# Kernel optimization log

Measured on AMD Instinct MI355X. Metric: run time of the kernel, lower is better.

The kernel has to match this reference:

```python
import jax, jax.numpy as jnp
import numpy as np

N = 50000      # total packed nodes
E = 1600000    # edges (no self loops; layers add them)
G = 64         # graphs in the batch
F_IN = 24      # raw node feature dim
D = 64         # hidden dim
H = 4          # attention heads
C = D // H     # 16 channels per head
L = 3          # GAT layers
NEG = 0.2      # LeakyReLU negative slope (GATv2 default)
EPS = 1e-5     # LayerNorm eps


def setup_inputs() -> dict:
    key = jax.random.key(0)
    ks = jax.random.split(key, 16)
    x = jax.random.normal(ks[0], (N, F_IN), jnp.float32)
    src = jax.random.randint(ks[1], (E,), 0, N)
    dst = jax.random.randint(ks[2], (E,), 0, N)
    dst = jnp.where(dst == src, (dst + 1) % N, dst)  # keep edge list self-loop free
    edge_index = jnp.stack([src, dst]).astype(jnp.int32)
    batch = jnp.sort(jax.random.randint(ks[3], (N,), 0, G)).astype(jnp.int32)
    s = 0.1
    return dict(
        x=x, edge_index=edge_index, batch=batch,
        w_in=jax.random.normal(ks[4], (F_IN, D), jnp.float32) * s,
        b_in=jnp.zeros((D,), jnp.float32),
        w_l=jax.random.normal(ks[5], (L, D, D), jnp.float32) * s,
        b_l=jnp.zeros((L, D), jnp.float32),
        w_r=jax.random.normal(ks[6], (L, D, D), jnp.float32) * s,
        b_r=jnp.zeros((L, D), jnp.float32),
        att=jax.random.normal(ks[7], (L, H, C), jnp.float32) * s,
        b_gat=jnp.zeros((L, D), jnp.float32),
        ln_g=jnp.ones((L, D), jnp.float32),
        ln_b=jnp.zeros((L, D), jnp.float32),
        w_g1=jax.random.normal(ks[8], (D, D // 2), jnp.float32) * s,
        b_g1=jnp.zeros((D // 2,), jnp.float32),
        w_g2=jax.random.normal(ks[9], (D // 2, 1), jnp.float32) * s,
        b_g2=jnp.zeros((1,), jnp.float32),
        w_out=jax.random.normal(ks[10], (D, D), jnp.float32) * s,
        b_out=jnp.zeros((D,), jnp.float32),
    )


def _layernorm(h, g, b):
    m = h.mean(-1, keepdims=True)
    v = ((h - m) ** 2).mean(-1, keepdims=True)
    return (h - m) * jax.lax.rsqrt(v + EPS) * g + b


def _gatv2(h, src, dst, wl, bl, wr, br, att, bg):
    n = h.shape[0]
    xl = (h @ wl + bl).reshape(n, H, C)   # source transform
    xr = (h @ wr + br).reshape(n, H, C)   # target transform
    # edge scores: att . leaky_relu(xl[j] + xr[i])  -> [E', H]
    e = jnp.sum(jax.nn.leaky_relu(xl[src] + xr[dst], NEG) * att, axis=-1)
    emax = jax.ops.segment_max(e, dst, num_segments=n)
    ex = jnp.exp(e - emax[dst])
    denom = jax.ops.segment_sum(ex, dst, num_segments=n)
    alpha = ex / denom[dst]               # segment softmax over incoming edges
    out = jax.ops.segment_sum(alpha[:, :, None] * xl[src], dst, num_segments=n)
    return out.reshape(n, D) + bg


def reference(x, edge_index, batch, w_in, b_in, w_l, b_l, w_r, b_r, att, b_gat,
              ln_g, ln_b, w_g1, b_g1, w_g2, b_g2, w_out, b_out):
    n = x.shape[0]
    loops = jnp.arange(n, dtype=edge_index.dtype)
    src = jnp.concatenate([edge_index[0], loops])  # add self loops once
    dst = jnp.concatenate([edge_index[1], loops])
    h = jax.nn.relu(x @ w_in + b_in)
    for i in range(L):
        res = h
        h = _gatv2(h, src, dst, w_l[i], b_l[i], w_r[i], b_r[i], att[i], b_gat[i])
        h = _layernorm(h + res, ln_g[i], ln_b[i])
        if i < L - 1:
            h = jax.nn.relu(h)
    # GlobalAttention pooling: gate MLP -> per-graph softmax -> weighted sum
    gate = jax.nn.relu(h @ w_g1 + b_g1) @ w_g2 + b_g2  # [N, 1]
    gmax = jax.ops.segment_max(gate, batch, num_segments=G)
    ge = jnp.exp(gate - gmax[batch])
    gs = jax.ops.segment_sum(ge, batch, num_segments=G)
    a = ge / jnp.where(gs > 0, gs, 1.0)[batch]
    emb = jax.ops.segment_sum(a * h, batch, num_segments=G)  # [G, D]
    return jax.nn.relu(emb @ w_out + b_out)
```

## Files before the change

### kernel.cpp

```cpp
#include <hip/hip_runtime.h>

#define NEGS   0.2f
#define LN_EPS 1e-5f
#define BSH    7
#define BN     128
#define TILE   4096
#define LOG2E  1.44269504f

typedef const float* __restrict__ fp;
typedef _Float16 v2h __attribute__((ext_vector_type(2)));
typedef _Float16 v8h __attribute__((ext_vector_type(8)));
typedef float    v4f __attribute__((ext_vector_type(4)));

__device__ __forceinline__ v2h u2h(unsigned u){ union{unsigned u; v2h h;} c; c.u = u; return c.h; }
__device__ __forceinline__ unsigned h2u(v2h h){ union{v2h h; unsigned u;} c; c.h = h; return c.u; }

template<int CTRL>
__device__ __forceinline__ float dppadd(float x){
  int y = __builtin_amdgcn_update_dpp(0, __float_as_int(x), CTRL, 0xF, 0xF, true);
  return x + __int_as_float(y);
}
__device__ __forceinline__ float hsum8(float s){
  s = dppadd<0xB1>(s);
  s = dppadd<0x4E>(s);
  s = dppadd<0x141>(s);
  return s;
}
__device__ __forceinline__ float edge_w(v2h v, v2h xrv, v2h att2, float negm8){
  v2h t = v + xrv;
  t = __builtin_elementwise_max(t, t * (_Float16)NEGS);
  float s = hsum8(__builtin_amdgcn_fdot2(t, att2, negm8, false));
  return __builtin_amdgcn_exp2f(s);
}

__global__ __launch_bounds__(256) void k_in(fp x, fp w, fp b, float* __restrict__ h,
                                            unsigned* __restrict__ h16, int N){
  __shared__ float ws[24*64];
  __shared__ float bs[64];
  __shared__ float xs[4][24];
  int tid = threadIdx.x;
  for (int i = tid; i < 24*64; i += 256) ws[i] = w[i];
  if (tid < 64) bs[tid] = b[tid];
  int r = tid >> 6, c = tid & 63;
  int row = blockIdx.x*4 + r;
  if (c < 24 && row < N) xs[r][c] = x[row*24 + c];
  __syncthreads();
  float acc = bs[c];
  #pragma unroll
  for (int k = 0; k < 24; ++k) acc = fmaf(xs[r][k], ws[k*64 + c], acc);
  float y = fmaxf(acc, 0.f);
  float y1 = __shfl_down(y, 1);
  if (row < N){
    h[(size_t)row*64 + c] = y;
    if (!(c & 1)){
      v2h p; p.x = (_Float16)y; p.y = (_Float16)y1;
      h16[(size_t)row*32 + (c >> 1)] = h2u(p);
    }
  }
}

__global__ __launch_bounds__(256) void k_wprep(fp w_l, fp w_r, _Float16* __restrict__ wf){
  int lm = blockIdx.x;
  const float* src = ((lm & 1) ? w_r : w_l) + (lm >> 1)*4096;
  _Float16* dst = wf + lm*4096;
  for (int d = threadIdx.x; d < 4096; d += 256){
    int j = d & 7, l = (d >> 3) & 63, kc = (d >> 9) & 1, nt = d >> 10;
    int k = kc*32 + (l >> 4)*8 + j;
    int n = nt*16 + (l & 15);
    dst[d] = (_Float16)src[k*64 + n];
  }
}

__global__ __launch_bounds__(256) void t_hist(const int* __restrict__ dstA, int* __restrict__ counts,
                                              int E, int K, int ntiles){
  __shared__ int hist[512];
  int t = blockIdx.x, tid = threadIdx.x;
  for (int i = tid; i < K; i += 256) hist[i] = 0;
  __syncthreads();
  int e0 = t*TILE, e1 = min(e0 + TILE, E);
  for (int e = e0 + tid; e < e1; e += 256)
    atomicAdd(&hist[dstA[e] >> BSH], 1);
  __syncthreads();
  for (int i = tid; i < K; i += 256) counts[i*ntiles + t] = hist[i];
}

__global__ __launch_bounds__(512) void s_scan_tiles(int* __restrict__ counts, int* __restrict__ btotal,
                                                    int ntiles){
  __shared__ int s[512];
  int b = blockIdx.x, tid = threadIdx.x;
  int v = (tid < ntiles) ? counts[b*ntiles + tid] : 0;
  s[tid] = v;
  __syncthreads();
  for (int off = 1; off < 512; off <<= 1){
    int t = (tid >= off) ? s[tid - off] : 0;
    __syncthreads();
    s[tid] += t;
    __syncthreads();
  }
  if (tid < ntiles) counts[b*ntiles + tid] = s[tid] - v;
  if (tid == 511) btotal[b] = s[511];
}

__global__ __launch_bounds__(512) void s_scan_buckets(const int* __restrict__ btotal,
                                                      int* __restrict__ bbase, int K, int E){
  __shared__ int s[512];
  int tid = threadIdx.x;
  int v = (tid < K) ? btotal[tid] : 0;
  s[tid] = v;
  __syncthreads();
  for (int off = 1; off < 512; off <<= 1){
    int t = (tid >= off) ? s[tid - off] : 0;
    __syncthreads();
    s[tid] += t;
    __syncthreads();
  }
  if (tid < K) bbase[tid] = s[tid] - v;
  if (tid == 0) bbase[K] = E;
}

__global__ __launch_bounds__(256) void t_scatter(const int* __restrict__ srcA, const int* __restrict__ dstA,
                                                 const int* __restrict__ counts, const int* __restrict__ bbase,
                                                 unsigned* __restrict__ packed, int E, int K, int ntiles){
  __shared__ int gb[512];
  __shared__ int cur[512];
  int t = blockIdx.x, tid = threadIdx.x;
  for (int i = tid; i < K; i += 256){
    gb[i] = bbase[i] + counts[i*ntiles + t];
    cur[i] = 0;
  }
  __syncthreads();
  int e0 = t*TILE, e1 = min(e0 + TILE, E);
  for (int e = e0 + tid; e < e1; e += 256){
    int d = dstA[e], sv = srcA[e];
    int b = d >> BSH;
    int p = atomicAdd(&cur[b], 1);
    packed[gb[b] + p] = ((unsigned)(d & (BN-1)) << 25) | (unsigned)sv;
  }
}

__global__ __launch_bounds__(256) void k_fine(const unsigned* __restrict__ packed, const int* __restrict__ bbase,
                                              int* __restrict__ row_ptr, int* __restrict__ col, int N, int K){
  __shared__ int hist[BN];
  __shared__ int excl[BN];
  int b = blockIdx.x, tid = threadIdx.x;
  int node0 = b << BSH;
  int e_base = bbase[b], e_end = bbase[b+1];
  if (tid < BN) hist[tid] = 0;
  __syncthreads();
  for (int e = e_base + tid; e < e_end; e += 256)
    atomicAdd(&hist[packed[e] >> 25], 1);
  __syncthreads();
  int v = (tid < BN) ? hist[tid] : 0;
  if (tid < BN) excl[tid] = v;
  __syncthreads();
  for (int off = 1; off < BN; off <<= 1){
    int t2 = 0;
    if (tid < BN && tid >= off) t2 = excl[tid - off];
    __syncthreads();
    if (tid < BN) excl[tid] += t2;
    __syncthreads();
  }
  int nn = min(BN, N - node0);
  if (tid < nn) row_ptr[node0 + tid] = e_base + excl[tid] - v;
  if (b == K-1 && tid == 0) row_ptr[N] = e_end;
  if (tid < BN) hist[tid] = excl[tid] - v;
  __syncthreads();
  for (int e = e_base + tid; e < e_end; e += 256){
    unsigned u = packed[e];
    int dl = u >> 25;
    int p = atomicAdd(&hist[dl], 1);
    col[e_base + p] = (int)(u & 0x1FFFFFFu);
  }
}

__global__ __launch_bounds__(256) void k_xfm(const unsigned* __restrict__ h16,
                                             const _Float16* __restrict__ wf,
                                             fp blg, fp brg,
                                             unsigned* __restrict__ xl16, unsigned* __restrict__ xr16, int N){
  int tid = threadIdx.x, wave = tid >> 6, lane = tid & 63;
  int quad = lane >> 4, ln = lane & 15;
  int m0 = blockIdx.x*64 + wave*16;
  if (m0 >= N) return;
  int m = m0 + ln;
  bool mv = m < N;
  v8h a0 = {}, a1 = {};
  if (mv){
    a0 = *(const v8h*)&h16[(size_t)m*32 + quad*4];
    a1 = *(const v8h*)&h16[(size_t)m*32 + 16 + quad*4];
  }
  #pragma unroll
  for (int mat = 0; mat < 2; ++mat){
    const _Float16* wb = wf + mat*4096;
    fp bias = mat ? brg : blg;
    unsigned* dst = mat ? xr16 : xl16;
    #pragma unroll
    for (int nt = 0; nt < 4; ++nt){
      v8h b0 = *(const v8h*)&wb[nt*1024 + lane*8];
      v8h b1 = *(const v8h*)&wb[nt*1024 + 512 + lane*8];
      float bv = bias[nt*16 + ln];
      v4f acc = {bv, bv, bv, bv};
      acc = __builtin_amdgcn_mfma_f32_16x16x32_f16(a0, b0, acc, 0, 0, 0);
      acc = __builtin_amdgcn_mfma_f32_16x16x32_f16(a1, b1, acc, 0, 0, 0);
      #pragma unroll
      for (int r = 0; r < 4; ++r){
        float partner = __shfl_xor(acc[r], 1);
        int node = m0 + quad*4 + r;
        if (!(lane & 1) && node < N){
          v2h p; p.x = (_Float16)acc[r]; p.y = (_Float16)partner;
          dst[(size_t)node*32 + nt*8 + (ln >> 1)] = h2u(p);
        }
      }
    }
  }
}

__global__ __launch_bounds__(256) void k_gat(const unsigned* __restrict__ xl16, const unsigned* __restrict__ xr16,
                                             float* __restrict__ h, unsigned* __restrict__ h16,
                                             const int* __restrict__ row_ptr, const int* __restrict__ col,
                                             fp att, fp bg, fp lng, fp lnb, int N, int do_relu){
  int lane = threadIdx.x & 63;
  int node = blockIdx.x*4 + (threadIdx.x >> 6);
  if (node >= N) return;
  int l = lane & 31;
  bool lower = lane < 32;
  int off = lower ? 0 : 1;
  v2h att2; att2.x = (_Float16)(att[2*l] * LOG2E); att2.y = (_Float16)(att[2*l+1] * LOG2E);
  v2h xrv = u2h(xr16[(size_t)node*32 + l]);
  v2h xlv = u2h(xl16[(size_t)node*32 + l]);
  v2h ts = xlv + xrv;
  ts = __builtin_elementwise_max(ts, ts * (_Float16)NEGS);
  const float m = hsum8(__builtin_amdgcn_fdot2(ts, att2, 0.f, false));
  const float negm8 = m * -0.125f;
  float den0 = lower ? 1.f : 0.f, den1 = 0.f, den2 = 0.f, den3 = 0.f;
  float a0x = lower ? (float)xlv.x : 0.f, a0y = lower ? (float)xlv.y : 0.f;
  float a1x = 0.f, a1y = 0.f, a2x = 0.f, a2y = 0.f, a3x = 0.f, a3y = 0.f;
  int e = row_ptr[node], e1 = row_ptr[node+1];
  for (; e + 8 <= e1; e += 8){
    int j0 = col[e+off], j1 = col[e+2+off], j2 = col[e+4+off], j3 = col[e+6+off];
    v2h v0 = u2h(xl16[(size_t)j0*32 + l]);
    v2h v1 = u2h(xl16[(size_t)j1*32 + l]);
    v2h v2 = u2h(xl16[(size_t)j2*32 + l]);
    v2h v3 = u2h(xl16[(size_t)j3*32 + l]);
    float w0 = edge_w(v0, xrv, att2, negm8);
    float w1 = edge_w(v1, xrv, att2, negm8);
    float w2 = edge_w(v2, xrv, att2, negm8);
    float w3 = edge_w(v3, xrv, att2, negm8);
    den0 += w0; a0x = fmaf(w0, (float)v0.x, a0x); a0y = fmaf(w0, (float)v0.y, a0y);
    den1 += w1; a1x = fmaf(w1, (float)v1.x, a1x); a1y = fmaf(w1, (float)v1.y, a1y);
    den2 += w2; a2x = fmaf(w2, (float)v2.x, a2x); a2y = fmaf(w2, (float)v2.y, a2y);
    den3 += w3; a3x = fmaf(w3, (float)v3.x, a3x); a3y = fmaf(w3, (float)v3.y, a3y);
  }
  for (; e + 2 <= e1; e += 2){
    int j0 = col[e+off];
    v2h v0 = u2h(xl16[(size_t)j0*32 + l]);
    float w0 = edge_w(v0, xrv, att2, negm8);
    den0 += w0; a0x = fmaf(w0, (float)v0.x, a0x); a0y = fmaf(w0, (float)v0.y, a0y);
  }
  if (e < e1){
    int j0 = col[e];
    v2h v0 = u2h(xl16[(size_t)j0*32 + l]);
    float w0 = edge_w(v0, xrv, att2, negm8);
    if (!lower) w0 = 0.f;
    den0 += w0; a0x = fmaf(w0, (float)v0.x, a0x); a0y = fmaf(w0, (float)v0.y, a0y);
  }
  float den = (den0 + den1) + (den2 + den3);
  float ax = (a0x + a1x) + (a2x + a3x);
  float ay = (a0y + a1y) + (a2y + a3y);
  den += __shfl_xor(den, 32);
  ax  += __shfl_xor(ax, 32);
  ay  += __shfl_xor(ay, 32);
  float inv = 1.f / den;
  float2 bg2 = *(const float2*)&bg[2*l];
  float2 h2  = *(const float2*)&h[(size_t)node*64 + 2*l];
  float ox = ax*inv + bg2.x + h2.x;
  float oy = ay*inv + bg2.y + h2.y;
  float sl = ox + oy;
  #pragma unroll
  for (int o = 1; o < 32; o <<= 1) sl += __shfl_xor(sl, o);
  float mean = sl * (1.f/64.f);
  float dx = ox - mean, dy = oy - mean;
  float vsl = dx*dx + dy*dy;
  #pragma unroll
  for (int o = 1; o < 32; o <<= 1) vsl += __shfl_xor(vsl, o);
  float rs = rsqrtf(vsl * (1.f/64.f) + LN_EPS);
  float2 lg2 = *(const float2*)&lng[2*l];
  float2 lb2 = *(const float2*)&lnb[2*l];
  float yx = dx*rs*lg2.x + lb2.x;
  float yy = dy*rs*lg2.y + lb2.y;
  if (do_relu){ yx = fmaxf(yx, 0.f); yy = fmaxf(yy, 0.f); }
  if (lower){
    float2 y2; y2.x = yx; y2.y = yy;
    *(float2*)&h[(size_t)node*64 + 2*l] = y2;
    v2h p; p.x = (_Float16)yx; p.y = (_Float16)yy;
    h16[(size_t)node*32 + l] = h2u(p);
  }
}

__global__ __launch_bounds__(256) void k_gate(const float* __restrict__ h, fp w1, fp b1, fp w2, fp b2,
                                              float* __restrict__ gate, int N){
  __shared__ float w1s[2048];
  __shared__ float hrow[16][64];
  int tid = threadIdx.x;
  for (int i = tid*4; i < 2048; i += 1024) *(float4*)&w1s[i] = *(const float4*)&w1[i];
  int base = blockIdx.x*16;
  int nrows = min(16, N - base);
  int lim = nrows*64;
  for (int i = tid*4; i < lim; i += 1024)
    *(float4*)&hrow[0][i] = *(const float4*)&h[(size_t)base*64 + i];
  __syncthreads();
  int wave = tid >> 6, lane = tid & 63;
  int j = lane & 31, half = lane >> 5;
  float b1v = b1[j], w2v = w2[j], b2v = b2[0];
  int k0 = half*32;
  #pragma unroll
  for (int it = 0; it < 4; ++it){
    int r = wave*4 + it;
    int node = base + r;
    if (node >= N) break;
    float s = 0.f;
    #pragma unroll 8
    for (int k = k0; k < k0 + 32; ++k) s = fmaf(hrow[r][k], w1s[k*32 + j], s);
    s += __shfl_xor(s, 32);
    float hid = fmaxf(s + b1v, 0.f);
    float contrib = (half == 0) ? hid * w2v : 0.f;
    #pragma unroll
    for (int o = 1; o < 64; o <<= 1) contrib += __shfl_xor(contrib, o);
    if (lane == 0) gate[node] = contrib + b2v;
  }
}

__global__ __launch_bounds__(256) void k_gmax(const float* __restrict__ gate, const int* __restrict__ batch,
                                              float* __restrict__ gmax, float* __restrict__ gsum,
                                              float* __restrict__ embsum, int N){
  int g = blockIdx.x, tid = threadIdx.x;
  if (tid < 64) embsum[g*64 + tid] = 0.f;
  if (tid == 64) gsum[g] = 0.f;
  int lo = 0, hi = N;
  while (lo < hi){ int mid = (lo + hi) >> 1; if (batch[mid] < g) lo = mid + 1; else hi = mid; }
  int start = lo;
  hi = N;
  while (lo < hi){ int mid = (lo + hi) >> 1; if (batch[mid] < g + 1) lo = mid + 1; else hi = mid; }
  int end = lo;
  float m = -3.4e38f;
  for (int i = start + tid; i < end; i += 256) m = fmaxf(m, gate[i]);
  #pragma unroll
  for (int o = 1; o < 64; o <<= 1) m = fmaxf(m, __shfl_xor(m, o));
  __shared__ float ws[4];
  if ((tid & 63) == 0) ws[tid >> 6] = m;
  __syncthreads();
  if (tid == 0) gmax[g] = fmaxf(fmaxf(ws[0], ws[1]), fmaxf(ws[2], ws[3]));
}

__global__ __launch_bounds__(256) void k_emb(const float* __restrict__ h, const float* __restrict__ gate,
                                             const int* __restrict__ batch, const float* __restrict__ gmax,
                                             float* __restrict__ gsum, float* __restrict__ embsum, int N){
  int lane = threadIdx.x & 63;
  int wv = blockIdx.x*4 + (threadIdx.x >> 6);
  int s = wv*64;
  if (s >= N) return;
  int e = min(s + 64, N);
  int cur = batch[s];
  float gm = gmax[cur];
  float acc = 0.f, asum = 0.f;
  for (int i = s; i < e; ++i){
    int g = batch[i];
    if (g != cur){
      atomicAdd(&embsum[cur*64 + lane], acc);
      if (lane == 0) atomicAdd(&gsum[cur], asum);
      acc = 0.f; asum = 0.f; cur = g; gm = gmax[g];
    }
    float a = __expf(gate[i] - gm);
    acc = fmaf(a, h[(size_t)i*64 + lane], acc);
    asum += a;
  }
  atomicAdd(&embsum[cur*64 + lane], acc);
  if (lane == 0) atomicAdd(&gsum[cur], asum);
}

__global__ __launch_bounds__(64) void k_out(const float* __restrict__ embsum, const float* __restrict__ gsum,
                                            fp w_out, fp b_out, float* __restrict__ out, int G){
  int g = blockIdx.x, lane = threadIdx.x;
  __shared__ float emb[64];
  float gs = gsum[g];
  float inv = (gs > 0.f) ? 1.f/gs : 1.f;
  emb[lane] = embsum[g*64 + lane] * inv;
  __syncthreads();
  float o2 = b_out[lane];
  #pragma unroll 8
  for (int d = 0; d < 64; ++d) o2 = fmaf(emb[d], w_out[d*64 + lane], o2);
  out[g*64 + lane] = fmaxf(o2, 0.f);
}

extern "C" void kernel_launch(void* const* d_in, const int* in_sizes, int n_in,
                              void* d_out, int out_size, void* d_ws, size_t ws_size,
                              hipStream_t stream) {
  const int N = in_sizes[0] / 24;
  const int E = in_sizes[1] / 2;
  const int G = out_size / 64;
  const int K = (N + BN - 1) >> BSH;
  const int ntiles = (E + TILE - 1) / TILE;

  fp x      = (fp)d_in[0];
  const int* edge  = (const int*)d_in[1];
  const int* batch = (const int*)d_in[2];
  fp w_in   = (fp)d_in[3];
  fp b_in   = (fp)d_in[4];
  fp w_l    = (fp)d_in[5];
  fp b_l    = (fp)d_in[6];
  fp w_r    = (fp)d_in[7];
  fp b_r    = (fp)d_in[8];
  fp att    = (fp)d_in[9];
  fp b_gat  = (fp)d_in[10];
  fp ln_g   = (fp)d_in[11];
  fp ln_b   = (fp)d_in[12];
  fp w_g1   = (fp)d_in[13];
  fp b_g1   = (fp)d_in[14];
  fp w_g2   = (fp)d_in[15];
  fp b_g2   = (fp)d_in[16];
  fp w_out  = (fp)d_in[17];
  fp b_out  = (fp)d_in[18];
  float* out = (float*)d_out;

  char* wp = (char*)d_ws;
  auto alloc = [&](size_t bytes) -> char* {
    char* p = wp; wp += (bytes + 255) & ~(size_t)255; return p;
  };
  float*    h       = (float*)    alloc((size_t)N*64*sizeof(float));
  unsigned* h16     = (unsigned*) alloc((size_t)N*32*sizeof(unsigned));
  unsigned* xl16    = (unsigned*) alloc((size_t)N*32*sizeof(unsigned));
  unsigned* xr16    = (unsigned*) alloc((size_t)N*32*sizeof(unsigned));
  int*      col     = (int*)      alloc((size_t)E*sizeof(int));
  unsigned* packed  = (unsigned*) alloc((size_t)E*sizeof(unsigned));
  int*      counts  = (int*)      alloc((size_t)K*ntiles*sizeof(int));
  int*      btotal  = (int*)      alloc((size_t)K*sizeof(int));
  int*      bbase   = (int*)      alloc((size_t)(K+1)*sizeof(int));
  int*      row_ptr = (int*)      alloc((size_t)(N+1)*sizeof(int));
  float*    gate    = (float*)    alloc((size_t)N*sizeof(float));
  float*    gmax    = (float*)    alloc((size_t)G*sizeof(float));
  float*    gsum    = (float*)    alloc((size_t)(G + G*64)*sizeof(float));
  float*    embsum  = gsum + G;
  _Float16* wf      = (_Float16*) alloc((size_t)3*2*4096*sizeof(_Float16));

  const int* srcA = edge;
  const int* dstA = edge + E;

  k_in<<<(N + 3)/4, 256, 0, stream>>>(x, w_in, b_in, h, h16, N);
  k_wprep<<<6, 256, 0, stream>>>(w_l, w_r, wf);

  t_hist<<<ntiles, 256, 0, stream>>>(dstA, counts, E, K, ntiles);
  s_scan_tiles<<<K, 512, 0, stream>>>(counts, btotal, ntiles);
  s_scan_buckets<<<1, 512, 0, stream>>>(btotal, bbase, K, E);
  t_scatter<<<ntiles, 256, 0, stream>>>(srcA, dstA, counts, bbase, packed, E, K, ntiles);
  k_fine<<<K, 256, 0, stream>>>(packed, bbase, row_ptr, col, N, K);

  for (int i = 0; i < 3; ++i){
    k_xfm<<<(N + 63)/64, 256, 0, stream>>>(h16, wf + i*8192, b_l + i*64, b_r + i*64,
                                           xl16, xr16, N);
    k_gat<<<(N + 3)/4, 256, 0, stream>>>(xl16, xr16, h, h16, row_ptr, col,
                                         att + i*64, b_gat + i*64, ln_g + i*64, ln_b + i*64,
                                         N, i < 2 ? 1 : 0);
  }
  k_gate<<<(N + 15)/16, 256, 0, stream>>>(h, w_g1, b_g1, w_g2, b_g2, gate, N);
  k_gmax<<<G, 256, 0, stream>>>(gate, batch, gmax, gsum, embsum, N);
  k_emb<<<(N + 255)/256, 256, 0, stream>>>(h, gate, batch, gmax, gsum, embsum, N);
  k_out<<<G, 64, 0, stream>>>(embsum, gsum, w_out, b_out, out, G);
}
```

Before: 384.9 us.

## Fuse prologue kernels, merge scans, and fuse gate pooling into one pass

The input projection, per-tile destination histogram, weight fp16 repacking and zeroing of pooling accumulators are merged into one launch that branches on block index. The two prefix-scan kernels become one, where the last block to finish (found through an atomic counter) does the bucket scan. The gate MLP, per-graph max and weighted embedding sum become one kernel that reuses the h rows already in shared memory and drops the max subtraction from the softmax. Fewer launches and less global traffic are the aim; the risks are possible exp overflow for large gates and reliance on threadfence plus the atomic counter being correct for the scan handoff.

After: 486.5 us. +26.4%, slower.

```diff
diff --git a/kernel.cpp b/kernel.cpp
--- a/kernel.cpp
+++ b/kernel.cpp
@@ -33,60 +33,67 @@
   return __builtin_amdgcn_exp2f(s);
 }
 
-__global__ __launch_bounds__(256) void k_in(fp x, fp w, fp b, float* __restrict__ h,
-                                            unsigned* __restrict__ h16, int N){
-  __shared__ float ws[24*64];
-  __shared__ float bs[64];
-  __shared__ float xs[4][24];
-  int tid = threadIdx.x;
-  for (int i = tid; i < 24*64; i += 256) ws[i] = w[i];
-  if (tid < 64) bs[tid] = b[tid];
-  int r = tid >> 6, c = tid & 63;
-  int row = blockIdx.x*4 + r;
-  if (c < 24 && row < N) xs[r][c] = x[row*24 + c];
-  __syncthreads();
-  float acc = bs[c];
-  #pragma unroll
-  for (int k = 0; k < 24; ++k) acc = fmaf(xs[r][k], ws[k*64 + c], acc);
-  float y = fmaxf(acc, 0.f);
-  float y1 = __shfl_down(y, 1);
-  if (row < N){
-    h[(size_t)row*64 + c] = y;
-    if (!(c & 1)){
-      v2h p; p.x = (_Float16)y; p.y = (_Float16)y1;
-      h16[(size_t)row*32 + (c >> 1)] = h2u(p);
+__global__ __launch_bounds__(256) void f_in_hist(fp x, fp w, fp b, float* __restrict__ h,
+                                                 unsigned* __restrict__ h16,
+                                                 const int* __restrict__ dstA, int* __restrict__ counts,
+                                                 float* __restrict__ zbuf, int zn, int* __restrict__ ctr,
+                                                 fp w_l, fp w_r, _Float16* __restrict__ wf,
+                                                 int N, int E, int K, int ntiles, int NB_IN){
+  __shared__ __align__(16) float sm[1700];
+  int bid = blockIdx.x, tid = threadIdx.x;
+  if (bid < NB_IN){
+    float* ws = sm;
+    float* bs = sm + 1536;
+    float* xs = sm + 1600;
+    for (int i = tid; i < 1536; i += 256) ws[i] = w[i];
+    if (tid < 64) bs[tid] = b[tid];
+    int r = tid >> 6, c = tid & 63;
+    int row = bid*4 + r;
+    if (c < 24 && row < N) xs[r*24 + c] = x[row*24 + c];
+    __syncthreads();
+    float acc = bs[c];
+    #pragma unroll
+    for (int k = 0; k < 24; ++k) acc = fmaf(xs[r*24 + k], ws[k*64 + c], acc);
+    float y = fmaxf(acc, 0.f);
+    float y1 = __shfl_down(y, 1);
+    if (row < N){
+      h[(size_t)row*64 + c] = y;
+      if (!(c & 1)){
+        v2h p; p.x = (_Float16)y; p.y = (_Float16)y1;
+        h16[(size_t)row*32 + (c >> 1)] = h2u(p);
+      }
     }
-  }
-}
-
-__global__ __launch_bounds__(256) void k_wprep(fp w_l, fp w_r, _Float16* __restrict__ wf){
-  int lm = blockIdx.x;
-  const float* src = ((lm & 1) ? w_r : w_l) + (lm >> 1)*4096;
-  _Float16* dst = wf + lm*4096;
-  for (int d = threadIdx.x; d < 4096; d += 256){
-    int j = d & 7, l = (d >> 3) & 63, kc = (d >> 9) & 1, nt = d >> 10;
-    int k = kc*32 + (l >> 4)*8 + j;
-    int n = nt*16 + (l & 15);
-    dst[d] = (_Float16)src[k*64 + n];
-  }
-}
-
-__global__ __launch_bounds__(256) void t_hist(const int* __restrict__ dstA, int* __restrict__ counts,
-                                              int E, int K, int ntiles){
-  __shared__ int hist[512];
-  int t = blockIdx.x, tid = threadIdx.x;
-  for (int i = tid; i < K; i += 256) hist[i] = 0;
-  __syncthreads();
-  int e0 = t*TILE, e1 = min(e0 + TILE, E);
-  for (int e = e0 + tid; e < e1; e += 256)
-    atomicAdd(&hist[dstA[e] >> BSH], 1);
-  __syncthreads();
-  for (int i = tid; i < K; i += 256) counts[i*ntiles + t] = hist[i];
-}
-
-__global__ __launch_bounds__(512) void s_scan_tiles(int* __restrict__ counts, int* __restrict__ btotal,
-                                                    int ntiles){
+  } else if (bid < NB_IN + ntiles){
+    int* hist = (int*)sm;
+    int t = bid - NB_IN;
+    for (int i = tid; i < K; i += 256) hist[i] = 0;
+    __syncthreads();
+    int e0 = t*TILE, e1 = min(e0 + TILE, E);
+    for (int e = e0 + tid; e < e1; e += 256)
+      atomicAdd(&hist[dstA[e] >> BSH], 1);
+    __syncthreads();
+    for (int i = tid; i < K; i += 256) counts[i*ntiles + t] = hist[i];
+  } else if (bid == NB_IN + ntiles){
+    for (int i = tid; i < zn; i += 256) zbuf[i] = 0.f;
+    if (tid == 0) ctr[0] = 0;
+  } else {
+    int lm = bid - NB_IN - ntiles - 1;
+    const float* src = ((lm & 1) ? w_r : w_l) + (lm >> 1)*4096;
+    _Float16* dst = wf + lm*4096;
+    for (int d = tid; d < 4096; d += 256){
+      int j = d & 7, l = (d >> 3) & 63, kc = (d >> 9) & 1, nt = d >> 10;
+      int k = kc*32 + (l >> 4)*8 + j;
+      int n = nt*16 + (l & 15);
+      dst[d] = (_Float16)src[k*64 + n];
+    }
+  }
+}
+
+__global__ __launch_bounds__(512) void s_scan(int* __restrict__ counts, int* __restrict__ btotal,
+                                              int* __restrict__ bbase, int* __restrict__ ctr,
+                                              int K, int E, int ntiles){
   __shared__ int s[512];
+  __shared__ int isLast;
   int b = blockIdx.x, tid = threadIdx.x;
   int v = (tid < ntiles) ? counts[b*ntiles + tid] : 0;
   s[tid] = v;
@@ -99,14 +106,14 @@
   }
   if (tid < ntiles) counts[b*ntiles + tid] = s[tid] - v;
   if (tid == 511) btotal[b] = s[511];
-}
-
-__global__ __launch_bounds__(512) void s_scan_buckets(const int* __restrict__ btotal,
-                                                      int* __restrict__ bbase, int K, int E){
-  __shared__ int s[512];
-  int tid = threadIdx.x;
-  int v = (tid < K) ? btotal[tid] : 0;
-  s[tid] = v;
+  __threadfence();
+  __syncthreads();
+  if (tid == 0){ int old = atomicAdd(ctr, 1); isLast = (old == (int)gridDim.x - 1) ? 1 : 0; }
+  __syncthreads();
+  if (!isLast) return;
+  __threadfence();
+  int v2 = (tid < K) ? btotal[tid] : 0;
+  s[tid] = v2;
   __syncthreads();
   for (int off = 1; off < 512; off <<= 1){
     int t = (tid >= off) ? s[tid - off] : 0;
@@ -114,7 +121,7 @@
     s[tid] += t;
     __syncthreads();
   }
-  if (tid < K) bbase[tid] = s[tid] - v;
+  if (tid < K) bbase[tid] = s[tid] - v2;
   if (tid == 0) bbase[K] = E;
 }
 
@@ -296,10 +303,12 @@
   }
 }
 
-__global__ __launch_bounds__(256) void k_gate(const float* __restrict__ h, fp w1, fp b1, fp w2, fp b2,
-                                              float* __restrict__ gate, int N){
+__global__ __launch_bounds__(256) void k_gate_emb(const float* __restrict__ h, fp w1, fp b1, fp w2, fp b2,
+                                                  const int* __restrict__ batch,
+                                                  float* __restrict__ gsum, float* __restrict__ embsum, int N){
   __shared__ float w1s[2048];
   __shared__ float hrow[16][64];
+  __shared__ float gates[16];
   int tid = threadIdx.x;
   for (int i = tid*4; i < 2048; i += 1024) *(float4*)&w1s[i] = *(const float4*)&w1[i];
   int base = blockIdx.x*16;
@@ -315,8 +324,7 @@
   #pragma unroll
   for (int it = 0; it < 4; ++it){
     int r = wave*4 + it;
-    int node = base + r;
-    if (node >= N) break;
+    if (r >= nrows) break;
     float s = 0.f;
     #pragma unroll 8
     for (int k = k0; k < k0 + 32; ++k) s = fmaf(hrow[r][k], w1s[k*32 + j], s);
@@ -325,56 +333,28 @@
     float contrib = (half == 0) ? hid * w2v : 0.f;
     #pragma unroll
     for (int o = 1; o < 64; o <<= 1) contrib += __shfl_xor(contrib, o);
-    if (lane == 0) gate[node] = contrib + b2v;
-  }
-}
-
-__global__ __launch_bounds__(256) void k_gmax(const float* __restrict__ gate, const int* __restrict__ batch,
-                                              float* __restrict__ gmax, float* __restrict__ gsum,
-                                              float* __restrict__ embsum, int N){
-  int g = blockIdx.x, tid = threadIdx.x;
-  if (tid < 64) embsum[g*64 + tid] = 0.f;
-  if (tid == 64) gsum[g] = 0.f;
-  int lo = 0, hi = N;
-  while (lo < hi){ int mid = (lo + hi) >> 1; if (batch[mid] < g) lo = mid + 1; else hi = mid; }
-  int start = lo;
-  hi = N;
-  while (lo < hi){ int mid = (lo + hi) >> 1; if (batch[mid] < g + 1) lo = mid + 1; else hi = mid; }
-  int end = lo;
-  float m = -3.4e38f;
-  for (int i = start + tid; i < end; i += 256) m = fmaxf(m, gate[i]);
-  #pragma unroll
-  for (int o = 1; o < 64; o <<= 1) m = fmaxf(m, __shfl_xor(m, o));
-  __shared__ float ws[4];
-  if ((tid & 63) == 0) ws[tid >> 6] = m;
-  __syncthreads();
-  if (tid == 0) gmax[g] = fmaxf(fmaxf(ws[0], ws[1]), fmaxf(ws[2], ws[3]));
-}
-
-__global__ __launch_bounds__(256) void k_emb(const float* __restrict__ h, const float* __restrict__ gate,
-                                             const int* __restrict__ batch, const float* __restrict__ gmax,
-                                             float* __restrict__ gsum, float* __restrict__ embsum, int N){
-  int lane = threadIdx.x & 63;
-  int wv = blockIdx.x*4 + (threadIdx.x >> 6);
-  int s = wv*64;
-  if (s >= N) return;
-  int e = min(s + 64, N);
-  int cur = batch[s];
-  float gm = gmax[cur];
-  float acc = 0.f, asum = 0.f;
-  for (int i = s; i < e; ++i){
-    int g = batch[i];
-    if (g != cur){
-      atomicAdd(&embsum[cur*64 + lane], acc);
-      if (lane == 0) atomicAdd(&gsum[cur], asum);
-      acc = 0.f; asum = 0.f; cur = g; gm = gmax[g];
+    if (lane == 0) gates[r] = contrib + b2v;
+  }
+  __syncthreads();
+  int s0 = base + wave*4;
+  if (s0 < N){
+    int e = min(s0 + 4, N);
+    int cur = batch[s0];
+    float acc = 0.f, asum = 0.f;
+    for (int i = s0; i < e; ++i){
+      int g = batch[i];
+      if (g != cur){
+        atomicAdd(&embsum[cur*64 + lane], acc);
+        if (lane == 0) atomicAdd(&gsum[cur], asum);
+        acc = 0.f; asum = 0.f; cur = g;
+      }
+      float a = __expf(gates[i - base]);
+      acc = fmaf(a, hrow[i - base][lane], acc);
+      asum += a;
     }
-    float a = __expf(gate[i] - gm);
-    acc = fmaf(a, h[(size_t)i*64 + lane], acc);
-    asum += a;
-  }
-  atomicAdd(&embsum[cur*64 + lane], acc);
-  if (lane == 0) atomicAdd(&gsum[cur], asum);
+    atomicAdd(&embsum[cur*64 + lane], acc);
+    if (lane == 0) atomicAdd(&gsum[cur], asum);
+  }
 }
 
 __global__ __launch_bounds__(64) void k_out(const float* __restrict__ embsum, const float* __restrict__ gsum,
@@ -399,6 +379,7 @@
   const int G = out_size / 64;
   const int K = (N + BN - 1) >> BSH;
   const int ntiles = (E + TILE - 1) / TILE;
+  const int NB_IN = (N + 3) / 4;
 
   fp x      = (fp)d_in[0];
   const int* edge  = (const int*)d_in[1];
@@ -435,21 +416,19 @@
   int*      btotal  = (int*)      alloc((size_t)K*sizeof(int));
   int*      bbase   = (int*)      alloc((size_t)(K+1)*sizeof(int));
   int*      row_ptr = (int*)      alloc((size_t)(N+1)*sizeof(int));
-  float*    gate    = (float*)    alloc((size_t)N*sizeof(float));
-  float*    gmax    = (float*)    alloc((size_t)G*sizeof(float));
   float*    gsum    = (float*)    alloc((size_t)(G + G*64)*sizeof(float));
   float*    embsum  = gsum + G;
   _Float16* wf      = (_Float16*) alloc((size_t)3*2*4096*sizeof(_Float16));
+  int*      ctr     = (int*)      alloc(256);
 
   const int* srcA = edge;
   const int* dstA = edge + E;
-
-  k_in<<<(N + 3)/4, 256, 0, stream>>>(x, w_in, b_in, h, h16, N);
-  k_wprep<<<6, 256, 0, stream>>>(w_l, w_r, wf);
-
-  t_hist<<<ntiles, 256, 0, stream>>>(dstA, counts, E, K, ntiles);
-  s_scan_tiles<<<K, 512, 0, stream>>>(counts, btotal, ntiles);
-  s_scan_buckets<<<1, 512, 0, stream>>>(btotal, bbase, K, E);
+  const int zn = G + G*64;
+
+  f_in_hist<<<NB_IN + ntiles + 7, 256, 0, stream>>>(x, w_in, b_in, h, h16, dstA, counts,
+                                                    gsum, zn, ctr, w_l, w_r, wf,
+                                                    N, E, K, ntiles, NB_IN);
+  s_scan<<<K, 512, 0, stream>>>(counts, btotal, bbase, ctr, K, E, ntiles);
   t_scatter<<<ntiles, 256, 0, stream>>>(srcA, dstA, counts, bbase, packed, E, K, ntiles);
   k_fine<<<K, 256, 0, stream>>>(packed, bbase, row_ptr, col, N, K);
 
@@ -460,8 +439,6 @@
                                          att + i*64, b_gat + i*64, ln_g + i*64, ln_b + i*64,
                                          N, i < 2 ? 1 : 0);
   }
-  k_gate<<<(N + 15)/16, 256, 0, stream>>>(h, w_g1, b_g1, w_g2, b_g2, gate, N);
-  k_gmax<<<G, 256, 0, stream>>>(gate, batch, gmax, gsum, embsum, N);
-  k_emb<<<(N + 255)/256, 256, 0, stream>>>(h, gate, batch, gmax, gsum, embsum, N);
+  k_gate_emb<<<(N + 15)/16, 256, 0, stream>>>(h, w_g1, b_g1, w_g2, b_g2, batch, gsum, embsum, N);
   k_out<<<G, 64, 0, stream>>>(embsum, gsum, w_out, b_out, out, G);
 }
```
